# Performance work log

Hardware: AMD Instinct MI355X
Metric: run time of the kernel (lower is better)

## Reference

```python
import jax, jax.numpy as jnp
import numpy as np
import math

# Constants matching init_kwargs
H = 16            # num_attention_heads
K = 8             # tisa_num_kernels
NUM_AGNOSTIC = 2  # num_position_agnostic_heads
MAX_FV = 512.0
MIN_FV = 8.0
P_EPS = 1e-8
EPS = 1e-8


def _slopes():
    # ALiBi-like geometric slope schedule from the module __init__ (non-learned buffer)
    first = -math.log(P_EPS) / (MIN_FV / 2.0)
    last = -math.log(P_EPS) / (MAX_FV / 2.0)
    aware = H - NUM_AGNOSTIC
    s = first * (last / first) ** (jnp.arange(H, dtype=jnp.float32) / (aware - 1))
    # position-agnostic heads get zero slope
    return s * (jnp.arange(H) < aware).astype(jnp.float32)


def setup_inputs() -> dict:
    key = jax.random.key(0)
    ks = jax.random.split(key, 5)
    B, L, D = 4, 1024, 64
    q = jax.random.normal(ks[0], (B, H, L, D), jnp.float32)
    k = jax.random.normal(ks[1], (B, H, L, D), jnp.float32)
    v = jax.random.normal(ks[2], (B, H, L, D), jnp.float32)
    offsets = jax.random.normal(ks[3], (1, K, H, 1, 1), jnp.float32) * 15.0
    amplitudes = jax.random.normal(ks[4], (1, K, H, 1, 1), jnp.float32) * 0.01
    sharpness = jnp.full((1, K, H, 1, 1), 5.0, jnp.float32)
    bias_param = jnp.ones((1, H, 1, 1), jnp.float32)
    return {"q": q, "k": k, "v": v, "offsets": offsets, "amplitudes": amplitudes,
            "sharpness": sharpness, "bias_param": bias_param}


def reference(q, k, v, offsets, amplitudes, sharpness, bias_param):
    B, Hh, L, D = q.shape
    rel = jnp.arange(-L + 1, L, dtype=q.dtype)            # (2L-1,) relative positions
    slopes = _slopes()                                     # (H,)
    exp_decay = -jnp.abs(rel)[None, :] * slopes[:, None]   # (H, 2L-1)

    off = offsets.reshape(K, Hh, 1)
    amp = amplitudes.reshape(K, Hh, 1)
    sh = sharpness.reshape(K, Hh, 1)
    # sigmoid kernel per (kernel, head, relpos); eval mode -> no dropout
    kernel = jnp.abs(amp) * jax.nn.sigmoid(jnp.sign(amp) * ((rel[None, None, :] - off) / sh))
    ksum = kernel.sum(axis=0)                              # (H, 2L-1)
    bias_rel = jnp.log(ksum + EPS + bias_param.reshape(Hh, 1))
    rel_bias = bias_rel + exp_decay                        # (H, 2L-1)

    # relative -> absolute: bias[i, j] = rel_bias[j - i + L - 1]
    idx = jnp.arange(L)[None, :] - jnp.arange(L)[:, None] + (L - 1)  # (L, L)
    attn_bias = rel_bias[:, idx]                           # (H, L, L)

    scale = 1.0 / jnp.sqrt(jnp.asarray(D, q.dtype))
    scores = jnp.einsum('bhqd,bhkd->bhqk', q, k) * scale + attn_bias[None]
    probs = jax.nn.softmax(scores, axis=-1)
    return jnp.einsum('bhqk,bhkd->bhqd', probs, v)
```

## Files before the change

kernel.cpp:

```cpp
#include <hip/hip_runtime.h>
#include <math.h>

#define Bq 4
#define Hh 16
#define Lq 1024
#define Dd 64
#define Kk 8
#define QT 128
#define KT 128
#define SRk 72
#define SRv 136
#define TB 1152
#define FMAX 8.0f
#define LOG2E 1.44269504f

#define KBUF (KT * SRk * 2)
#define VBUF (Dd * SRv * 2)
#define BOFF (2 * (KBUF + VBUF))
#define SMEM_BYTES (BOFF + 2 * TB * 4)

typedef __attribute__((ext_vector_type(8))) short short8;
typedef __attribute__((ext_vector_type(4))) unsigned int u32x4;
typedef __attribute__((ext_vector_type(16))) float f32x16;

__device__ __forceinline__ unsigned int pk2(float a, float b) {
    return __builtin_amdgcn_perm(__float_as_uint(b) + 0x8000u,
                                 __float_as_uint(a) + 0x8000u,
                                 0x07060302u);
}

__device__ __forceinline__ int jperm(int j) {
    return (j & 32) | ((j & 8) << 1) | ((j & 4) << 1) | ((j & 16) >> 2) | (j & 3);
}

__global__ __launch_bounds__(512, 2) void attn_kernel(
    const float* __restrict__ qp, const float* __restrict__ kp,
    const float* __restrict__ vp,
    const float* __restrict__ off, const float* __restrict__ amp,
    const float* __restrict__ sh, const float* __restrict__ bpar,
    float* __restrict__ out)
{
    __shared__ __align__(16) char smem[SMEM_BYTES];
    float* bias2 = (float*)(smem + BOFF);

    const int bh = blockIdx.x;
    const int qs = blockIdx.y * QT;
    const int t  = threadIdx.x;
    const int w  = t >> 6;
    const int qw = w >> 1;
    const int sw = w & 1;
    const int lane = t & 63;
    const int l31 = lane & 31;
    const int h5  = lane >> 5;
    const int h   = bh & 15;

    float slope = (h < Hh - 2) ? 4.605170185988092f * exp2f(-6.0f * (float)h / 13.0f) : 0.0f;
    #pragma unroll
    for (int it = 0; it < 3; ++it) {
        int i = it * 512 + t;
        if (i < TB - 1) {
            float rel = (float)(i - 127 - qs);
            float ksum = 0.0f;
            #pragma unroll
            for (int kk = 0; kk < Kk; ++kk) {
                float a = amp[kk * Hh + h];
                float o = off[kk * Hh + h];
                float s = sh[kk * Hh + h];
                float sgn = (a > 0.0f) ? 1.0f : ((a < 0.0f) ? -1.0f : 0.0f);
                ksum += fabsf(a) / (1.0f + __expf(-sgn * (rel - o) / s));
            }
            bias2[i] = (logf(ksum + 1e-8f + bpar[h]) - fabsf(rel) * slope - FMAX) * LOG2E;
        }
    }

    const float QS = 0.125f * LOG2E;
    short8 bq[4];
    const float* qrow = qp + ((size_t)bh * Lq + qs + 32 * qw + l31) * Dd;
    #pragma unroll
    for (int c = 0; c < 4; ++c) {
        float4 x0 = *(const float4*)(qrow + c * 16 + h5 * 8);
        float4 x1 = *(const float4*)(qrow + c * 16 + h5 * 8 + 4);
        u32x4 a;
        a[0] = pk2(x0.x * QS, x0.y * QS);
        a[1] = pk2(x0.z * QS, x0.w * QS);
        a[2] = pk2(x1.x * QS, x1.y * QS);
        a[3] = pk2(x1.z * QS, x1.w * QS);
        bq[c] = __builtin_bit_cast(short8, a);
    }

    const int g  = t >> 4;
    const int cl = t & 15;
    const int c4 = 4 * cl;
    const int jrow = 4 * g;
    const int vcb = 64 * (g >> 4) + jperm(jrow & 63);
    const float* kbase = kp + (size_t)bh * Lq * Dd;
    const float* vbase = vp + (size_t)bh * Lq * Dd;

    float4 kr[4], vr[4];
    #pragma unroll
    for (int u = 0; u < 4; ++u) {
        kr[u] = *(const float4*)(kbase + (size_t)(jrow + u) * Dd + c4);
        vr[u] = *(const float4*)(vbase + (size_t)(jrow + u) * Dd + c4);
    }

    __syncthreads();

    #pragma unroll
    for (int it = 0; it < 3; ++it) {
        int i = it * 512 + t;
        if (i < TB)
            bias2[TB + i] = bias2[i + 1 <= TB - 2 ? i + 1 : TB - 2];
    }
    {
        short* kw = (short*)(smem);
        short* vw = (short*)(smem + 2 * KBUF);
        #pragma unroll
        for (int u = 0; u < 4; ++u) {
            uint2 kv;
            kv.x = pk2(kr[u].x, kr[u].y);
            kv.y = pk2(kr[u].z, kr[u].w);
            *(uint2*)&kw[(jrow + u) * SRk + c4] = kv;
        }
        #pragma unroll
        for (int cc = 0; cc < 4; ++cc) {
            int d = c4 + cc;
            uint2 vv;
            vv.x = pk2(((const float*)&vr[0])[cc], ((const float*)&vr[1])[cc]);
            vv.y = pk2(((const float*)&vr[2])[cc], ((const float*)&vr[3])[cc]);
            *(uint2*)&vw[d * SRv + (vcb ^ (8 * ((d >> 3) & 7)))] = vv;
        }
    }
    __syncthreads();

    f32x16 O0, O1;
    #pragma unroll
    for (int r = 0; r < 16; ++r) { O0[r] = 0.f; O1[r] = 0.f; }
    float l_part = 0.0f;

    const int L0 = 4 * h5 - 32 * qw - l31 + 127;
    const int phi = L0 & 1;
    const float* bcopy = bias2 + phi * TB - phi;

    #pragma unroll 1
    for (int kt = 0; kt < Lq / KT; ++kt) {
        const int ks = kt * KT;
        const int cur = kt & 1;
        const short* kc = (const short*)(smem + cur * KBUF);
        const short* vc = (const short*)(smem + 2 * KBUF + cur * VBUF);

        if (kt < 7) {
            const float* kn = kbase + (size_t)(ks + KT) * Dd;
            const float* vn = vbase + (size_t)(ks + KT) * Dd;
            #pragma unroll
            for (int u = 0; u < 4; ++u) {
                kr[u] = *(const float4*)(kn + (size_t)(jrow + u) * Dd + c4);
                vr[u] = *(const float4*)(vn + (size_t)(jrow + u) * Dd + c4);
            }
        }

        f32x16 S0, S1;
        #pragma unroll
        for (int p = 0; p < 4; ++p) {
            int base0 = ks + 64 * sw + 8 * p + L0;
            float2 a0 = *(const float2*)(bcopy + base0);
            float2 a1 = *(const float2*)(bcopy + base0 + 2);
            float2 a2 = *(const float2*)(bcopy + base0 + 32);
            float2 a3 = *(const float2*)(bcopy + base0 + 34);
            S0[4 * p + 0] = a0.x; S0[4 * p + 1] = a0.y;
            S0[4 * p + 2] = a1.x; S0[4 * p + 3] = a1.y;
            S1[4 * p + 0] = a2.x; S1[4 * p + 1] = a2.y;
            S1[4 * p + 2] = a3.x; S1[4 * p + 3] = a3.y;
        }

        #pragma unroll
        for (int c = 0; c < 4; ++c) {
            short8 ak0 = *(const short8*)&kc[(64 * sw + l31) * SRk + c * 16 + h5 * 8];
            S0 = __builtin_amdgcn_mfma_f32_32x32x16_bf16(ak0, bq[c], S0, 0, 0, 0);
        }
        #pragma unroll
        for (int c = 0; c < 4; ++c) {
            short8 ak1 = *(const short8*)&kc[(64 * sw + 32 + l31) * SRk + c * 16 + h5 * 8];
            S1 = __builtin_amdgcn_mfma_f32_32x32x16_bf16(ak1, bq[c], S1, 0, 0, 0);
        }

        float lsum = 0.0f;
        #pragma unroll
        for (int r = 0; r < 16; ++r) {
            float e0 = __builtin_amdgcn_exp2f(S0[r]);
            float e1 = __builtin_amdgcn_exp2f(S1[r]);
            S0[r] = e0; S1[r] = e1;
            lsum += e0 + e1;
        }
        l_part += lsum;

        short8 ap[4];
        #pragma unroll
        for (int c = 0; c < 4; ++c) {
            int b = (c & 1) * 4;
            u32x4 a;
            if (c >> 1) {
                a[0] = pk2(S1[b + 0], S1[b + 1]);
                a[1] = pk2(S1[b + 2], S1[b + 3]);
                a[2] = pk2(S1[b + 8], S1[b + 9]);
                a[3] = pk2(S1[b + 10], S1[b + 11]);
            } else {
                a[0] = pk2(S0[b + 0], S0[b + 1]);
                a[1] = pk2(S0[b + 2], S0[b + 3]);
                a[2] = pk2(S0[b + 8], S0[b + 9]);
                a[3] = pk2(S0[b + 10], S0[b + 11]);
            }
            ap[c] = __builtin_bit_cast(short8, a);
        }

        #pragma unroll
        for (int nb = 0; nb < 2; ++nb) {
            int d = nb * 32 + l31;
            int swz = 8 * ((d >> 3) & 7);
            f32x16 acc = nb ? O1 : O0;
            #pragma unroll
            for (int c = 0; c < 4; ++c) {
                short8 bv = *(const short8*)&vc[d * SRv + 64 * sw + ((c * 16 + h5 * 8) ^ swz)];
                acc = __builtin_amdgcn_mfma_f32_32x32x16_bf16(ap[c], bv, acc, 0, 0, 0);
            }
            if (nb) O1 = acc; else O0 = acc;
        }

        if (kt < 7) {
            short* kw = (short*)(smem + (cur ^ 1) * KBUF);
            short* vw = (short*)(smem + 2 * KBUF + (cur ^ 1) * VBUF);
            #pragma unroll
            for (int u = 0; u < 4; ++u) {
                uint2 kv;
                kv.x = pk2(kr[u].x, kr[u].y);
                kv.y = pk2(kr[u].z, kr[u].w);
                *(uint2*)&kw[(jrow + u) * SRk + c4] = kv;
            }
            #pragma unroll
            for (int cc = 0; cc < 4; ++cc) {
                int d = c4 + cc;
                uint2 vv;
                vv.x = pk2(((const float*)&vr[0])[cc], ((const float*)&vr[1])[cc]);
                vv.y = pk2(((const float*)&vr[2])[cc], ((const float*)&vr[3])[cc]);
                *(uint2*)&vw[d * SRv + (vcb ^ (8 * ((d >> 3) & 7)))] = vv;
            }
        }
        __syncthreads();
    }

    l_part += __shfl_xor(l_part, 32);
    float* red = (float*)smem;
    const int rb = (w * 64 + lane) * 17;
    #pragma unroll
    for (int r = 0; r < 16; ++r) red[rb + r] = sw ? O0[r] : O1[r];
    red[rb + 16] = l_part;
    __syncthreads();
    const int pb = ((w ^ 1) * 64 + lane) * 17;
    float inv = 1.0f / (l_part + red[pb + 16]);
    float* ob = out + ((size_t)bh * Lq + qs + 32 * qw) * Dd;
    #pragma unroll
    for (int r = 0; r < 16; ++r) {
        float o = (sw ? O1[r] : O0[r]) + red[pb + r];
        int rowp = (r & 3) + 8 * (r >> 2) + 4 * h5;
        float invp = __shfl(inv, rowp, 32);
        ob[(size_t)rowp * Dd + 32 * sw + l31] = o * invp;
    }
}

extern "C" void kernel_launch(void* const* d_in, const int* in_sizes, int n_in,
                              void* d_out, int out_size, void* d_ws, size_t ws_size,
                              hipStream_t stream) {
    const float* q   = (const float*)d_in[0];
    const float* k   = (const float*)d_in[1];
    const float* v   = (const float*)d_in[2];
    const float* off = (const float*)d_in[3];
    const float* amp = (const float*)d_in[4];
    const float* sh  = (const float*)d_in[5];
    const float* bp  = (const float*)d_in[6];
    float* out = (float*)d_out;

    dim3 grid(Bq * Hh, Lq / QT);
    attn_kernel<<<grid, 512, 0, stream>>>(q, k, v, off, amp, sh, bp, out);
}
```

Before: 130.7 us.

## Pre-convert K/V to bf16 in a separate kernel and read MFMA operands directly from global

```diff
diff --git a/kernel.cpp b/kernel.cpp
--- a/kernel.cpp
+++ b/kernel.cpp
@@ -8,16 +8,9 @@
 #define Kk 8
 #define QT 128
 #define KT 128
-#define SRk 72
-#define SRv 136
 #define TB 1152
 #define FMAX 8.0f
 #define LOG2E 1.44269504f
-
-#define KBUF (KT * SRk * 2)
-#define VBUF (Dd * SRv * 2)
-#define BOFF (2 * (KBUF + VBUF))
-#define SMEM_BYTES (BOFF + 2 * TB * 4)
 
 typedef __attribute__((ext_vector_type(8))) short short8;
 typedef __attribute__((ext_vector_type(4))) unsigned int u32x4;
@@ -33,15 +26,49 @@
     return (j & 32) | ((j & 8) << 1) | ((j & 4) << 1) | ((j & 16) >> 2) | (j & 3);
 }
 
+__global__ __launch_bounds__(256) void conv_kernel(
+    const float* __restrict__ kp, const float* __restrict__ vp,
+    unsigned short* __restrict__ kb, unsigned short* __restrict__ vt)
+{
+    const int tid = blockIdx.x * 256 + threadIdx.x;
+    #pragma unroll
+    for (int it = 0; it < 2; ++it) {
+        const int n = (it * 262144 + tid) * 8;
+        float4 x0 = *(const float4*)(kp + n);
+        float4 x1 = *(const float4*)(kp + n + 4);
+        u32x4 a;
+        a[0] = pk2(x0.x, x0.y); a[1] = pk2(x0.z, x0.w);
+        a[2] = pk2(x1.x, x1.y); a[3] = pk2(x1.z, x1.w);
+        *(u32x4*)(kb + n) = a;
+    }
+    const int bh = tid >> 12;
+    const int dt = (tid >> 8) & 15;
+    const int jt = tid & 255;
+    const int j0 = 4 * jt;
+    const float* vsrc = vp + ((size_t)bh * Lq + j0) * Dd + 4 * dt;
+    float4 r0 = *(const float4*)(vsrc);
+    float4 r1 = *(const float4*)(vsrc + Dd);
+    float4 r2 = *(const float4*)(vsrc + 2 * Dd);
+    float4 r3 = *(const float4*)(vsrc + 3 * Dd);
+    const int slot = (j0 & ~63) | jperm(j0 & 63);
+    unsigned short* vd = vt + ((size_t)bh * Dd + 4 * dt) * Lq + slot;
+    uint2 w;
+    w.x = pk2(r0.x, r1.x); w.y = pk2(r2.x, r3.x); *(uint2*)(vd)          = w;
+    w.x = pk2(r0.y, r1.y); w.y = pk2(r2.y, r3.y); *(uint2*)(vd + Lq)     = w;
+    w.x = pk2(r0.z, r1.z); w.y = pk2(r2.z, r3.z); *(uint2*)(vd + 2 * Lq) = w;
+    w.x = pk2(r0.w, r1.w); w.y = pk2(r2.w, r3.w); *(uint2*)(vd + 3 * Lq) = w;
+}
+
 __global__ __launch_bounds__(512, 2) void attn_kernel(
-    const float* __restrict__ qp, const float* __restrict__ kp,
-    const float* __restrict__ vp,
+    const float* __restrict__ qp,
     const float* __restrict__ off, const float* __restrict__ amp,
     const float* __restrict__ sh, const float* __restrict__ bpar,
+    const unsigned short* __restrict__ kb,
+    const unsigned short* __restrict__ vt,
     float* __restrict__ out)
 {
-    __shared__ __align__(16) char smem[SMEM_BYTES];
-    float* bias2 = (float*)(smem + BOFF);
+    __shared__ __align__(16) float smem_f[8 * 64 * 17];
+    float* bias2 = smem_f;
 
     const int bh = blockIdx.x;
     const int qs = blockIdx.y * QT;
@@ -88,21 +115,6 @@
         bq[c] = __builtin_bit_cast(short8, a);
     }
 
-    const int g  = t >> 4;
-    const int cl = t & 15;
-    const int c4 = 4 * cl;
-    const int jrow = 4 * g;
-    const int vcb = 64 * (g >> 4) + jperm(jrow & 63);
-    const float* kbase = kp + (size_t)bh * Lq * Dd;
-    const float* vbase = vp + (size_t)bh * Lq * Dd;
-
-    float4 kr[4], vr[4];
-    #pragma unroll
-    for (int u = 0; u < 4; ++u) {
-        kr[u] = *(const float4*)(kbase + (size_t)(jrow + u) * Dd + c4);
-        vr[u] = *(const float4*)(vbase + (size_t)(jrow + u) * Dd + c4);
-    }
-
     __syncthreads();
 
     #pragma unroll
@@ -111,25 +123,6 @@
         if (i < TB)
             bias2[TB + i] = bias2[i + 1 <= TB - 2 ? i + 1 : TB - 2];
     }
-    {
-        short* kw = (short*)(smem);
-        short* vw = (short*)(smem + 2 * KBUF);
-        #pragma unroll
-        for (int u = 0; u < 4; ++u) {
-            uint2 kv;
-            kv.x = pk2(kr[u].x, kr[u].y);
-            kv.y = pk2(kr[u].z, kr[u].w);
-            *(uint2*)&kw[(jrow + u) * SRk + c4] = kv;
-        }
-        #pragma unroll
-        for (int cc = 0; cc < 4; ++cc) {
-            int d = c4 + cc;
-            uint2 vv;
-            vv.x = pk2(((const float*)&vr[0])[cc], ((const float*)&vr[1])[cc]);
-            vv.y = pk2(((const float*)&vr[2])[cc], ((const float*)&vr[3])[cc]);
-            *(uint2*)&vw[d * SRv + (vcb ^ (8 * ((d >> 3) & 7)))] = vv;
-        }
-    }
     __syncthreads();
 
     f32x16 O0, O1;
@@ -141,21 +134,23 @@
     const int phi = L0 & 1;
     const float* bcopy = bias2 + phi * TB - phi;
 
+    const unsigned short* kbb = kb + ((size_t)bh * Lq + 64 * sw + l31) * Dd + h5 * 8;
+    const unsigned short* vtb = vt + (size_t)bh * Dd * Lq + 64 * sw + h5 * 8;
+
     #pragma unroll 1
     for (int kt = 0; kt < Lq / KT; ++kt) {
         const int ks = kt * KT;
-        const int cur = kt & 1;
-        const short* kc = (const short*)(smem + cur * KBUF);
-        const short* vc = (const short*)(smem + 2 * KBUF + cur * VBUF);
-
-        if (kt < 7) {
-            const float* kn = kbase + (size_t)(ks + KT) * Dd;
-            const float* vn = vbase + (size_t)(ks + KT) * Dd;
-            #pragma unroll
-            for (int u = 0; u < 4; ++u) {
-                kr[u] = *(const float4*)(kn + (size_t)(jrow + u) * Dd + c4);
-                vr[u] = *(const float4*)(vn + (size_t)(jrow + u) * Dd + c4);
-            }
+
+        short8 ka0[4], ka1[4], vf0[4], vf1[4];
+        #pragma unroll
+        for (int c = 0; c < 4; ++c) {
+            ka0[c] = *(const short8*)(kbb + (size_t)ks * Dd + c * 16);
+            ka1[c] = *(const short8*)(kbb + (size_t)ks * Dd + 32 * Dd + c * 16);
+        }
+        #pragma unroll
+        for (int c = 0; c < 4; ++c) {
+            vf0[c] = *(const short8*)(vtb + (size_t)l31 * Lq + ks + c * 16);
+            vf1[c] = *(const short8*)(vtb + (size_t)(32 + l31) * Lq + ks + c * 16);
         }
 
         f32x16 S0, S1;
@@ -173,15 +168,11 @@
         }
 
         #pragma unroll
-        for (int c = 0; c < 4; ++c) {
-            short8 ak0 = *(const short8*)&kc[(64 * sw + l31) * SRk + c * 16 + h5 * 8];
-            S0 = __builtin_amdgcn_mfma_f32_32x32x16_bf16(ak0, bq[c], S0, 0, 0, 0);
-        }
-        #pragma unroll
-        for (int c = 0; c < 4; ++c) {
-            short8 ak1 = *(const short8*)&kc[(64 * sw + 32 + l31) * SRk + c * 16 + h5 * 8];
-            S1 = __builtin_amdgcn_mfma_f32_32x32x16_bf16(ak1, bq[c], S1, 0, 0, 0);
-        }
+        for (int c = 0; c < 4; ++c)
+            S0 = __builtin_amdgcn_mfma_f32_32x32x16_bf16(ka0[c], bq[c], S0, 0, 0, 0);
+        #pragma unroll
+        for (int c = 0; c < 4; ++c)
+            S1 = __builtin_amdgcn_mfma_f32_32x32x16_bf16(ka1[c], bq[c], S1, 0, 0, 0);
 
         float lsum = 0.0f;
         #pragma unroll
@@ -213,42 +204,16 @@
         }
 
         #pragma unroll
-        for (int nb = 0; nb < 2; ++nb) {
-            int d = nb * 32 + l31;
-            int swz = 8 * ((d >> 3) & 7);
-            f32x16 acc = nb ? O1 : O0;
-            #pragma unroll
-            for (int c = 0; c < 4; ++c) {
-                short8 bv = *(const short8*)&vc[d * SRv + 64 * sw + ((c * 16 + h5 * 8) ^ swz)];
-                acc = __builtin_amdgcn_mfma_f32_32x32x16_bf16(ap[c], bv, acc, 0, 0, 0);
-            }
-            if (nb) O1 = acc; else O0 = acc;
-        }
-
-        if (kt < 7) {
-            short* kw = (short*)(smem + (cur ^ 1) * KBUF);
-            short* vw = (short*)(smem + 2 * KBUF + (cur ^ 1) * VBUF);
-            #pragma unroll
-            for (int u = 0; u < 4; ++u) {
-                uint2 kv;
-                kv.x = pk2(kr[u].x, kr[u].y);
-                kv.y = pk2(kr[u].z, kr[u].w);
-                *(uint2*)&kw[(jrow + u) * SRk + c4] = kv;
-            }
-            #pragma unroll
-            for (int cc = 0; cc < 4; ++cc) {
-                int d = c4 + cc;
-                uint2 vv;
-                vv.x = pk2(((const float*)&vr[0])[cc], ((const float*)&vr[1])[cc]);
-                vv.y = pk2(((const float*)&vr[2])[cc], ((const float*)&vr[3])[cc]);
-                *(uint2*)&vw[d * SRv + (vcb ^ (8 * ((d >> 3) & 7)))] = vv;
-            }
-        }
-        __syncthreads();
-    }
-
+        for (int c = 0; c < 4; ++c)
+            O0 = __builtin_amdgcn_mfma_f32_32x32x16_bf16(ap[c], vf0[c], O0, 0, 0, 0);
+        #pragma unroll
+        for (int c = 0; c < 4; ++c)
+            O1 = __builtin_amdgcn_mfma_f32_32x32x16_bf16(ap[c], vf1[c], O1, 0, 0, 0);
+    }
+
+    __syncthreads();
     l_part += __shfl_xor(l_part, 32);
-    float* red = (float*)smem;
+    float* red = smem_f;
     const int rb = (w * 64 + lane) * 17;
     #pragma unroll
     for (int r = 0; r < 16; ++r) red[rb + r] = sw ? O0[r] : O1[r];
@@ -278,6 +243,11 @@
     const float* bp  = (const float*)d_in[6];
     float* out = (float*)d_out;
 
+    unsigned short* kb = (unsigned short*)d_ws;
+    unsigned short* vt = kb + (size_t)Bq * Hh * Lq * Dd;
+
+    conv_kernel<<<dim3(1024), 256, 0, stream>>>(k, v, kb, vt);
+
     dim3 grid(Bq * Hh, Lq / QT);
-    attn_kernel<<<grid, 512, 0, stream>>>(q, k, v, off, amp, sh, bp, out);
-}
+    attn_kernel<<<grid, 512, 0, stream>>>(q, off, amp, sh, bp, kb, vt, out);
+}
```

After: 181.5 us. 1.39x slower.
